# Kernel optimization log

Hardware: AMD Instinct MI355X
Metric: run time of the kernel (lower is better)

Reference implementation:

```python
import jax, jax.numpy as jnp
import numpy as np

EPS = 1e-5

def _layernorm(x, g, b):
    mu = jnp.mean(x, axis=-1, keepdims=True)
    var = jnp.mean((x - mu) ** 2, axis=-1, keepdims=True)
    return (x - mu) / jnp.sqrt(var + EPS) * g + b


def setup_inputs() -> dict:
    key = jax.random.key(0)
    ks = jax.random.split(key, 4)
    B, H, W, C = 8, 96, 96, 256
    return {
        "x1": jax.random.normal(ks[0], (B, H, W, C), dtype=jnp.float32),
        "x2": jax.random.normal(ks[1], (B, H, W, C), dtype=jnp.float32),
        # norm1 (shared LayerNorm applied to both x1 and x2)
        "g1": jnp.ones((C,), jnp.float32),
        "b1": jnp.zeros((C,), jnp.float32),
        # reprojection 1x1 conv: C -> 2C
        "Wr": jax.random.normal(ks[2], (2 * C, C), dtype=jnp.float32) * 0.05,
        "br": jnp.zeros((2 * C,), jnp.float32),
        # final LayerNorm over 2C
        "g2": jnp.ones((2 * C,), jnp.float32),
        "b2": jnp.zeros((2 * C,), jnp.float32),
        # learnable mixing scalars
        "a1": jnp.array(0.25, jnp.float32),
        "a2": jnp.array(0.25, jnp.float32),
        "a3": jnp.array(0.25, jnp.float32),
        "a4": jnp.array(0.25, jnpp_ := jnp.float32),
    }


def reference(x1, x2, g1, b1, Wr, br, g2, b2, a1, a2, a3, a4):
    B, H, W, C = x1.shape
    N, D = H * W, C  # head_count = 1, key_channels = value_channels = D
    n1 = _layernorm(x1.reshape(B, N, C), g1, b1)  # [B,N,D]
    n2 = _layernorm(x2.reshape(B, N, C), g1, b1)

    kq = jnp.swapaxes(n2, 1, 2)                   # [B,D,N]
    key_sm = jax.nn.softmax(kq, axis=2)           # softmax over N
    query = jax.nn.softmax(kq, axis=1)            # softmax over D
    value = jnp.swapaxes(n1, 1, 2)                # [B,D,N]

    # context = key @ value^T : [B,D,D]
    context = jnp.einsum('bdn,ben->bde', key_sm, value)

    def masked_softmax(k):
        # torch.topk + scatter mask == keep entries >= k-th largest per row
        thr = jax.lax.top_k(context, k)[0][..., -1:]
        return jax.nn.softmax(jnp.where(context >= thr, context, -jnp.inf), axis=-1)

    ks = [D // 2, (D * 2) // 3, (D * 3) // 4, (D * 4) // 5]
    o = [jnp.einsum('bde,ben->bdn', masked_softmax(k), query) for k in ks]
    att = a1 * o[0] + a2 * o[1] + a3 * o[2] + a4 * o[3]  # [B,D,N]

    # 1x1 conv reprojection D -> 2D, then LayerNorm over channels
    rep = jnp.einsum('oc,bcn->bno', Wr, att) + br         # [B,N,2D]
    rep = _layernorm(rep, g2, b2)
    # view(B,H,W,2C).permute(0,3,1,2)
    return jnp.transpose(rep.reshape(B, H, W, 2 * C), (0, 3, 1, 2))
```

## Files before the change

kernel.cpp:

```cpp
#include <hip/hip_runtime.h>
#include <hip/hip_bf16.h>

#define Bc 8
#define Nn 9216
#define Dd 256
#define Oo 512
#define EPSc 1e-5f

#define OFF_MU1    0
#define OFF_RSTD1  73728
#define OFF_MU2    147456
#define OFF_RSTD2  221184
#define OFF_ROWINV 294912
#define OFF_COLSUM 368640
#define OFF_M      370688
#define OFF_W2T    894976
#define OFF_CTXP   1419264

typedef __attribute__((ext_vector_type(4))) float f32x4;
typedef __attribute__((ext_vector_type(8))) short short8;
typedef __attribute__((ext_vector_type(8))) unsigned short ushort8;

static __device__ __forceinline__ unsigned short f2bf(float f) {
    __hip_bfloat16 h = __float2bfloat16(f);
    union { __hip_bfloat16 hh; unsigned short uu; } cv; cv.hh = h;
    return cv.uu;
}

#define SWZ(ch) (((((ch) >> 2) & 7)) ^ ((((ch) & 3)) << 1))

__global__ __launch_bounds__(256) void mg_k0_zero(float* __restrict__ p, int n4) {
    int i = blockIdx.x * 256 + threadIdx.x;
    if (i < n4) ((float4*)p)[i] = make_float4(0.f, 0.f, 0.f, 0.f);
}

__global__ __launch_bounds__(256) void mg_k1_stats(const float* __restrict__ x1, const float* __restrict__ x2,
                                                   const float* __restrict__ g1, const float* __restrict__ b1,
                                                   float* __restrict__ ws)
{
    float* mu1    = ws + OFF_MU1;
    float* rstd1  = ws + OFF_RSTD1;
    float* mu2    = ws + OFF_MU2;
    float* rstd2  = ws + OFF_RSTD2;
    float* rowinv = ws + OFF_ROWINV;
    float* colsum = ws + OFF_COLSUM;

    int t = threadIdx.x, lane = t & 63, w = t >> 6;
    int b = blockIdx.x / 144, rb = blockIdx.x % 144;
    int nbase = rb * 64;

    float4 g1v = ((const float4*)g1)[lane];
    float4 b1v = ((const float4*)b1)[lane];
    float cs0 = 0.f, cs1 = 0.f, cs2 = 0.f, cs3 = 0.f;
    __shared__ float csL[4][256];

    for (int i = 0; i < 16; ++i) {
        int n = nbase + i * 4 + w;
        int base = (b * Nn + n) * 64 + lane;
        float4 xa = ((const float4*)x1)[base];
        float4 xb = ((const float4*)x2)[base];
        float s1 = xa.x + xa.y + xa.z + xa.w;
        float q1 = xa.x*xa.x + xa.y*xa.y + xa.z*xa.z + xa.w*xa.w;
        float s2 = xb.x + xb.y + xb.z + xb.w;
        float q2 = xb.x*xb.x + xb.y*xb.y + xb.z*xb.z + xb.w*xb.w;
        #pragma unroll
        for (int m = 1; m < 64; m <<= 1) {
            s1 += __shfl_xor(s1, m); q1 += __shfl_xor(q1, m);
            s2 += __shfl_xor(s2, m); q2 += __shfl_xor(q2, m);
        }
        float m1 = s1 * (1.f / Dd), m2 = s2 * (1.f / Dd);
        float r1 = rsqrtf(q1 * (1.f / Dd) - m1 * m1 + EPSc);
        float r2 = rsqrtf(q2 * (1.f / Dd) - m2 * m2 + EPSc);
        int ni = b * Nn + n;
        if (lane == 0) { mu1[ni] = m1; rstd1[ni] = r1; mu2[ni] = m2; rstd2[ni] = r2; }
        float e0 = __expf((xb.x - m2) * r2 * g1v.x + b1v.x);
        float e1 = __expf((xb.y - m2) * r2 * g1v.y + b1v.y);
        float e2 = __expf((xb.z - m2) * r2 * g1v.z + b1v.z);
        float e3 = __expf((xb.w - m2) * r2 * g1v.w + b1v.w);
        float rs = e0 + e1 + e2 + e3;
        #pragma unroll
        for (int m = 1; m < 64; m <<= 1) rs += __shfl_xor(rs, m);
        if (lane == 0) rowinv[ni] = 1.f / rs;
        cs0 += e0; cs1 += e1; cs2 += e2; cs3 += e3;
    }
    csL[w][lane * 4 + 0] = cs0;
    csL[w][lane * 4 + 1] = cs1;
    csL[w][lane * 4 + 2] = cs2;
    csL[w][lane * 4 + 3] = cs3;
    __syncthreads();
    float tot = csL[0][t] + csL[1][t] + csL[2][t] + csL[3][t];
    atomicAdd(&colsum[b * Dd + t], tot);
}

__global__ __launch_bounds__(512, 2) void mg_k3_ctx(const float* __restrict__ x1, const float* __restrict__ x2,
                                                    const float* __restrict__ g1, const float* __restrict__ b1,
                                                    float* __restrict__ ws, int nks)
{
    __shared__ ushort PA[256 * 64];
    __shared__ ushort PB[256 * 64];
    const float* mu1   = ws + OFF_MU1;
    const float* rstd1 = ws + OFF_RSTD1;
    const float* mu2   = ws + OFF_MU2;
    const float* rstd2 = ws + OFF_RSTD2;
    float* ctxp = ws + OFF_CTXP;

    int t = threadIdx.x;
    int ks_i = blockIdx.x % nks;
    int b = blockIdx.x / nks;
    int krange = Nn / nks;
    int ntiles = krange >> 6;
    int n_base = ks_i * krange;

    int o  = t >> 6;
    int c4 = t & 63;

    f32x4 g1v = ((const f32x4*)g1)[c4];
    f32x4 b1v = ((const f32x4*)b1)[c4];

    int lane = t & 63, wave = t >> 6;
    int wd = wave & 3, we = wave >> 2;
    int l15 = lane & 15, kgrp = lane >> 4;

    f32x4 acc[4][8];
    #pragma unroll
    for (int dt = 0; dt < 4; ++dt)
        #pragma unroll
        for (int et = 0; et < 8; ++et) acc[dt][et] = (f32x4){0.f, 0.f, 0.f, 0.f};

    for (int st = 0; st < ntiles; ++st) {
        int rowb = b * Nn + n_base + st * 64 + o * 8;
        __syncthreads();
        {
            f32x4 mv0 = *(const f32x4*)(mu1 + rowb),   mv1 = *(const f32x4*)(mu1 + rowb + 4);
            f32x4 rv0 = *(const f32x4*)(rstd1 + rowb), rv1 = *(const f32x4*)(rstd1 + rowb + 4);
            float mva[8] = {mv0[0], mv0[1], mv0[2], mv0[3], mv1[0], mv1[1], mv1[2], mv1[3]};
            float rva[8] = {rv0[0], rv0[1], rv0[2], rv0[3], rv1[0], rv1[1], rv1[2], rv1[3]};
            f32x4 xv[8];
            #pragma unroll
            for (int rr = 0; rr < 8; ++rr)
                xv[rr] = ((const f32x4*)x1)[(size_t)(rowb + rr) * 64 + c4];
            #pragma unroll
            for (int i = 0; i < 4; ++i) {
                int ch = c4 * 4 + i;
                ushort8 u;
                #pragma unroll
                for (int rr = 0; rr < 8; ++rr)
                    u[rr] = f2bf((xv[rr][i] - mva[rr]) * rva[rr] * g1v[i] + b1v[i]);
                *(ushort8*)&PB[ch * 64 + ((o + SWZ(ch)) & 7) * 8] = u;
            }
        }
        {
            f32x4 mv0 = *(const f32x4*)(mu2 + rowb),   mv1 = *(const f32x4*)(mu2 + rowb + 4);
            f32x4 rv0 = *(const f32x4*)(rstd2 + rowb), rv1 = *(const f32x4*)(rstd2 + rowb + 4);
            float mva[8] = {mv0[0], mv0[1], mv0[2], mv0[3], mv1[0], mv1[1], mv1[2], mv1[3]};
            float rva[8] = {rv0[0], rv0[1], rv0[2], rv0[3], rv1[0], rv1[1], rv1[2], rv1[3]};
            f32x4 xv[8];
            #pragma unroll
            for (int rr = 0; rr < 8; ++rr)
                xv[rr] = ((const f32x4*)x2)[(size_t)(rowb + rr) * 64 + c4];
            #pragma unroll
            for (int i = 0; i < 4; ++i) {
                int ch = c4 * 4 + i;
                ushort8 u;
                #pragma unroll
                for (int rr = 0; rr < 8; ++rr)
                    u[rr] = f2bf(__expf((xv[rr][i] - mva[rr]) * rva[rr] * g1v[i] + b1v[i]));
                *(ushort8*)&PA[ch * 64 + ((o + SWZ(ch)) & 7) * 8] = u;
            }
        }
        __syncthreads();

        #pragma unroll
        for (int kk = 0; kk < 2; ++kk) {
            short8 af[4], bf[8];
            #pragma unroll
            for (int dt = 0; dt < 4; ++dt) {
                int ch = wd * 64 + dt * 16 + l15;
                af[dt] = *(const short8*)&PA[ch * 64 + (((kk << 2) + kgrp + SWZ(ch)) & 7) * 8];
            }
            #pragma unroll
            for (int et = 0; et < 8; ++et) {
                int ch = we * 128 + et * 16 + l15;
                bf[et] = *(const short8*)&PB[ch * 64 + (((kk << 2) + kgrp + SWZ(ch)) & 7) * 8];
            }
            #pragma unroll
            for (int dt = 0; dt < 4; ++dt)
                #pragma unroll
                for (int et = 0; et < 8; ++et)
                    acc[dt][et] = __builtin_amdgcn_mfma_f32_16x16x32_bf16(af[dt], bf[et], acc[dt][et], 0, 0, 0);
        }
    }

    size_t obase = ((size_t)ks_i * Bc + b) * (Dd * Dd);
    #pragma unroll
    for (int dt = 0; dt < 4; ++dt) {
        #pragma unroll
        for (int r = 0; r < 4; ++r) {
            int d = wd * 64 + dt * 16 + kgrp * 4 + r;
            float* rowp = ctxp + obase + (size_t)d * Dd + we * 128 + l15;
            #pragma unroll
            for (int et = 0; et < 8; ++et)
                rowp[et * 16] = acc[dt][et][r];
        }
    }
}

__global__ __launch_bounds__(256) void mg_k5_mask(const float* __restrict__ a1p, const float* __restrict__ a2p,
                                                  const float* __restrict__ a3p, const float* __restrict__ a4p,
                                                  float* __restrict__ ws, int nks)
{
    const float* ctxp   = ws + OFF_CTXP;
    const float* colsum = ws + OFF_COLSUM;
    float* Mo = ws + OFF_M;
    int t = threadIdx.x;
    int b = blockIdx.x >> 8, d = blockIdx.x & 255;
    __shared__ float s[256];
    __shared__ float wred[4][4];

    float c = 0.f;
    for (int p = 0; p < nks; ++p)
        c += ctxp[((size_t)p * Bc + b) * (Dd * Dd) + (size_t)d * Dd + t];
    float inv = 1.f / colsum[b * Dd + d];
    c *= inv;
    s[t] = c;
    __syncthreads();
    for (int k = 2; k <= 256; k <<= 1) {
        for (int j = k >> 1; j > 0; j >>= 1) {
            int ixj = t ^ j;
            if (ixj > t) {
                float A = s[t], Bv = s[ixj];
                bool desc = ((t & k) == 0);
                bool sw = desc ? (A < Bv) : (A > Bv);
                if (sw) { s[t] = Bv; s[ixj] = A; }
            }
            __syncthreads();
        }
    }
    float cmax = s[0];
    float t0 = s[127], t1 = s[169], t2 = s[191], t3 = s[203];
    float e = __expf(c - cmax);
    float w0 = (c >= t0) ? e : 0.f;
    float w1 = (c >= t1) ? e : 0.f;
    float w2 = (c >= t2) ? e : 0.f;
    float w3 = (c >= t3) ? e : 0.f;
    float v0 = w0, v1 = w1, v2 = w2, v3 = w3;
    #pragma unroll
    for (int m = 1; m < 64; m <<= 1) {
        v0 += __shfl_xor(v0, m); v1 += __shfl_xor(v1, m);
        v2 += __shfl_xor(v2, m); v3 += __shfl_xor(v3, m);
    }
    int lane = t & 63, wv = t >> 6;
    if (lane == 0) { wred[wv][0] = v0; wred[wv][1] = v1; wred[wv][2] = v2; wred[wv][3] = v3; }
    __syncthreads();
    float S0 = wred[0][0] + wred[1][0] + wred[2][0] + wred[3][0];
    float S1 = wred[0][1] + wred[1][1] + wred[2][1] + wred[3][1];
    float S2 = wred[0][2] + wred[1][2] + wred[2][2] + wred[3][2];
    float S3 = wred[0][3] + wred[1][3] + wred[2][3] + wred[3][3];
    float Mv = a1p[0] * (w0 / S0) + a2p[0] * (w1 / S1) + a3p[0] * (w2 / S2) + a4p[0] * (w3 / S3);
    Mo[(b * Dd + d) * Dd + t] = Mv;
}

__global__ __launch_bounds__(256) void mg_k6_w2(const float* __restrict__ Wr, float* __restrict__ ws)
{
    const float* Mo = ws + OFF_M;
    ushort* W2B = (ushort*)(ws + OFF_W2T);
    __shared__ float Mt[32][128];
    __shared__ float WrT[32][36];
    int t = threadIdx.x;
    int b = blockIdx.x >> 5, ob = (blockIdx.x >> 1) & 15, eh = blockIdx.x & 1;
    int o0 = ob * 32, e0 = eh * 128;
    int ol4 = t & 7, el = t >> 3;
    float acc[4][4];
    #pragma unroll
    for (int i = 0; i < 4; ++i)
        #pragma unroll
        for (int j = 0; j < 4; ++j) acc[i][j] = 0.f;

    for (int ch = 0; ch < 8; ++ch) {
        int c0 = ch * 32;
        __syncthreads();
        #pragma unroll
        for (int k = 0; k < 4; ++k) {
            int fi = t + k * 256;
            int row = fi >> 5, c4 = fi & 31;
            float4 mv = ((const float4*)Mo)[(b * Dd + c0 + row) * 64 + (e0 >> 2) + c4];
            *(float4*)&Mt[row][c4 * 4] = mv;
        }
        {
            int ol = t >> 3, c4 = t & 7;
            float4 wv = ((const float4*)Wr)[(o0 + ol) * 64 + (c0 >> 2) + c4];
            WrT[c4 * 4 + 0][ol] = wv.x;
            WrT[c4 * 4 + 1][ol] = wv.y;
            WrT[c4 * 4 + 2][ol] = wv.z;
            WrT[c4 * 4 + 3][ol] = wv.w;
        }
        __syncthreads();
        #pragma unroll
        for (int cc = 0; cc < 32; ++cc) {
            float4 w4 = *(const float4*)&WrT[cc][ol4 * 4];
            float4 m4 = *(const float4*)&Mt[cc][el * 4];
            float wv[4] = {w4.x, w4.y, w4.z, w4.w};
            float mv[4] = {m4.x, m4.y, m4.z, m4.w};
            #pragma unroll
            for (int i = 0; i < 4; ++i)
                #pragma unroll
                for (int j = 0; j < 4; ++j)
                    acc[i][j] = fmaf(wv[i], mv[j], acc[i][j]);
        }
    }
    {
        int e_base = e0 + el * 4;
        int ks = e_base >> 5;
        int kg = (e_base >> 3) & 3, jj = e_base & 7;
        #pragma unroll
        for (int i = 0; i < 4; ++i) {
            int o = o0 + ol4 * 4 + i;
            int wv2 = o >> 6, ot = (o >> 4) & 3, cA = o & 15;
            ushort4 u;
            u.x = f2bf(acc[i][0]); u.y = f2bf(acc[i][1]);
            u.z = f2bf(acc[i][2]); u.w = f2bf(acc[i][3]);
            size_t idx = ((size_t)b * 8 + ks) * 16384 + wv2 * 2048 + ot * 512
                       + (kg * 16 + cA) * 8 + jj;
            *(ushort4*)&W2B[idx] = u;
        }
    }
}

__global__ __launch_bounds__(512) void mg_k7_final(const float* __restrict__ x2,
        const float* __restrict__ g1, const float* __restrict__ b1,
        const float* __restrict__ br, const float* __restrict__ g2, const float* __restrict__ b2,
        const float* __restrict__ ws, float* __restrict__ out)
{
    __shared__ ushort smem[8192 + 2 * 16384];
    ushort* qsT = smem;
    ushort* W0 = smem + 8192;
    ushort* W1 = smem + 8192 + 16384;

    const float* mu2    = ws + OFF_MU2;
    const float* rstd2  = ws + OFF_RSTD2;
    const float* rowinv = ws + OFF_ROWINV;
    const ushort* W2B   = (const ushort*)(ws + OFF_W2T);

    int t = threadIdx.x;
    int b = blockIdx.x / 288, nt0 = blockIdx.x % 288;
    int n0 = nt0 * 32;
    int lw = t & 63, wave = t >> 6;
    int colA = lw & 15, kgrp = lw >> 4;

#define STAGEW(dstbuf, ksv)                                                        \
    {                                                                              \
        size_t so_ = ((size_t)b * 8 + (ksv)) * 16384 + wave * 2048;                \
        _Pragma("unroll")                                                          \
        for (int k_ = 0; k_ < 4; ++k_) {                                           \
            __builtin_amdgcn_global_load_lds(                                      \
                (const __attribute__((address_space(1))) unsigned int*)            \
                    (W2B + so_ + k_ * 512 + lw * 8),                               \
                (__attribute__((address_space(3))) unsigned int*)                  \
                    ((dstbuf) + wave * 2048 + k_ * 512),                           \
                16, 0, 0);                                                         \
        }                                                                          \
    }

    STAGEW(W0, 0);

    {
        int row = t >> 4, gpair = (t & 15) * 2;
        int ni = b * Nn + n0 + row;
        float m = mu2[ni], r = rstd2[ni], ri = rowinv[ni];
        #pragma unroll
        for (int jj = 0; jj < 2; ++jj) {
            int g = gpair + jj;
            const float4* xp = (const float4*)x2 + (size_t)ni * 64 + g * 2;
            float4 xa = xp[0], xb = xp[1];
            float4 ga = ((const float4*)g1)[g * 2], gc = ((const float4*)g1)[g * 2 + 1];
            float4 ba = ((const float4*)b1)[g * 2], bc = ((const float4*)b1)[g * 2 + 1];
            float v[8]  = {xa.x, xa.y, xa.z, xa.w, xb.x, xb.y, xb.z, xb.w};
            float gv[8] = {ga.x, ga.y, ga.z, ga.w, gc.x, gc.y, gc.z, gc.w};
            float bv[8] = {ba.x, ba.y, ba.z, ba.w, bc.x, bc.y, bc.z, bc.w};
            ushort8 u;
            #pragma unroll
            for (int q = 0; q < 8; ++q)
                u[q] = f2bf(__expf((v[q] - m) * r * gv[q] + bv[q]) * ri);
            *(ushort8*)&qsT[row * 256 + ((g ^ (row & 7)) << 3)] = u;
        }
    }
    __syncthreads();

    f32x4 acc[4][2];
    #pragma unroll
    for (int ot = 0; ot < 4; ++ot) {
        acc[ot][0] = (f32x4){0.f, 0.f, 0.f, 0.f};
        acc[ot][1] = (f32x4){0.f, 0.f, 0.f, 0.f};
    }

    #pragma unroll
    for (int ks = 0; ks < 8; ++ks) {
        if (ks < 7) {
            if ((ks & 1) == 0) { STAGEW(W1, ks + 1); }
            else               { STAGEW(W0, ks + 1); }
        }
        const ushort* wb = (ks & 1) ? W1 : W0;
        int gsl = ((ks * 4 + kgrp) ^ (colA & 7)) << 3;
        short8 bf0 = *(const short8*)&qsT[colA * 256 + gsl];
        short8 bf1 = *(const short8*)&qsT[(16 + colA) * 256 + gsl];
        #pragma unroll
        for (int ot = 0; ot < 4; ++ot) {
            short8 af = *(const short8*)&wb[wave * 2048 + ot * 512 + lw * 8];
            acc[ot][0] = __builtin_amdgcn_mfma_f32_16x16x32_bf16(af, bf0, acc[ot][0], 0, 0, 0);
            acc[ot][1] = __builtin_amdgcn_mfma_f32_16x16x32_bf16(af, bf1, acc[ot][1], 0, 0, 0);
        }
        __syncthreads();
    }
#undef STAGEW

    float (*stat)[2][16][2] = (float (*)[2][16][2])(void*)smem;
    float (*musig)[2] = (float (*)[2])((float*)(void*)smem + 512);

    float ps[2] = {0.f, 0.f}, pq[2] = {0.f, 0.f};
    #pragma unroll
    for (int ot = 0; ot < 4; ++ot) {
        #pragma unroll
        for (int r = 0; r < 4; ++r) {
            int o = wave * 64 + ot * 16 + kgrp * 4 + r;
            float bb = br[o];
            float v0 = acc[ot][0][r] + bb;
            float v1 = acc[ot][1][r] + bb;
            acc[ot][0][r] = v0; acc[ot][1][r] = v1;
            ps[0] += v0; pq[0] += v0 * v0;
            ps[1] += v1; pq[1] += v1 * v1;
        }
    }
    #pragma unroll
    for (int m = 16; m <= 32; m <<= 1) {
        ps[0] += __shfl_xor(ps[0], m); pq[0] += __shfl_xor(pq[0], m);
        ps[1] += __shfl_xor(ps[1], m); pq[1] += __shfl_xor(pq[1], m);
    }
    if (lw < 16) {
        stat[wave][0][lw][0] = ps[0]; stat[wave][0][lw][1] = pq[0];
        stat[wave][1][lw][0] = ps[1]; stat[wave][1][lw][1] = pq[1];
    }
    __syncthreads();
    if (t < 32) {
        int ntl = t >> 4, col = t & 15;
        float S = 0.f, Q = 0.f;
        #pragma unroll
        for (int w2 = 0; w2 < 8; ++w2) { S += stat[w2][ntl][col][0]; Q += stat[w2][ntl][col][1]; }
        float mu = S * (1.f / Oo);
        float var = Q * (1.f / Oo) - mu * mu;
        musig[t][0] = mu;
        musig[t][1] = rsqrtf(var + EPSc);
    }
    __syncthreads();

    float mn0 = musig[colA][0],      rs0 = musig[colA][1];
    float mn1 = musig[16 + colA][0], rs1 = musig[16 + colA][1];
    #pragma unroll
    for (int ot = 0; ot < 4; ++ot) {
        #pragma unroll
        for (int r = 0; r < 4; ++r) {
            int o = wave * 64 + ot * 16 + kgrp * 4 + r;
            float gg = g2[o], bb2 = b2[o];
            size_t ob = ((size_t)b * Oo + o) * Nn + n0;
            out[ob + colA]      = (acc[ot][0][r] - mn0) * rs0 * gg + bb2;
            out[ob + 16 + colA] = (acc[ot][1][r] - mn1) * rs1 * gg + bb2;
        }
    }
}

extern "C" void kernel_launch(void* const* d_in, const int* in_sizes, int n_in,
                              void* d_out, int out_size, void* d_ws, size_t ws_size,
                              hipStream_t stream)
{
    (void)in_sizes; (void)n_in; (void)out_size;
    const float* x1 = (const float*)d_in[0];
    const float* x2 = (const float*)d_in[1];
    const float* g1 = (const float*)d_in[2];
    const float* b1 = (const float*)d_in[3];
    const float* Wr = (const float*)d_in[4];
    const float* br = (const float*)d_in[5];
    const float* g2 = (const float*)d_in[6];
    const float* b2 = (const float*)d_in[7];
    const float* a1 = (const float*)d_in[8];
    const float* a2 = (const float*)d_in[9];
    const float* a3 = (const float*)d_in[10];
    const float* a4 = (const float*)d_in[11];
    float* ws = (float*)d_ws;
    float* out = (float*)d_out;

    const int cand[6] = {24, 16, 12, 8, 4, 2};
    int nks = 2;
    for (int ci = 0; ci < 6; ++ci) {
        if (((size_t)OFF_CTXP + (size_t)cand[ci] * 524288ull) * 4ull <= ws_size) { nks = cand[ci]; break; }
    }

    hipLaunchKernelGGL(mg_k0_zero, dim3(2), dim3(256), 0, stream, ws + OFF_COLSUM, 512);
    hipLaunchKernelGGL(mg_k1_stats, dim3(1152), dim3(256), 0, stream, x1, x2, g1, b1, ws);
    hipLaunchKernelGGL(mg_k3_ctx, dim3(Bc * nks), dim3(512), 0, stream, x1, x2, g1, b1, ws, nks);
    hipLaunchKernelGGL(mg_k5_mask, dim3(2048), dim3(256), 0, stream, a1, a2, a3, a4, ws, nks);
    hipLaunchKernelGGL(mg_k6_w2, dim3(256), dim3(256), 0, stream, Wr, ws);
    hipLaunchKernelGGL(mg_k7_final, dim3(2304), dim3(512), 0, stream, x2, g1, b1, br, g2, b2, ws, out);
}
```

Measured before the change: 191.1 us.

## Precompute bf16 normalized and exp tiles in stats kernel, feed ctx GEMM via LDS DMA

The stats kernel now also writes bf16 tiles of the normalized x1 and exp(normalized x2) into workspace, already in the swizzled LDS layout. A new context kernel loads these tiles straight into LDS with global_load_lds and runs the MFMA GEMM without recomputing normalization or exp from fp32 inputs. This removes the second fp32 read of x1/x2 and the per-element math from the ctx kernel. In exchange it writes and rereads about 75MB of bf16 intermediates, needs a larger workspace, and keeps the old path as a fallback.

```diff
diff --git a/kernel.cpp b/kernel.cpp
--- a/kernel.cpp
+++ b/kernel.cpp
@@ -16,6 +16,9 @@
 #define OFF_M      370688
 #define OFF_W2T    894976
 #define OFF_CTXP   1419264
+#define OFF_PNB    14002176
+#define OFF_PNA    23439360
+#define WS_FAST_END 32876544
 
 typedef __attribute__((ext_vector_type(4))) float f32x4;
 typedef __attribute__((ext_vector_type(8))) short short8;
@@ -34,10 +37,12 @@
     if (i < n4) ((float4*)p)[i] = make_float4(0.f, 0.f, 0.f, 0.f);
 }
 
-__global__ __launch_bounds__(256) void mg_k1_stats(const float* __restrict__ x1, const float* __restrict__ x2,
+__global__ __launch_bounds__(512) void mg_k1_stats(const float* __restrict__ x1, const float* __restrict__ x2,
                                                    const float* __restrict__ g1, const float* __restrict__ b1,
-                                                   float* __restrict__ ws)
+                                                   float* __restrict__ ws, int wp)
 {
+    __shared__ ushort Pls[16384];
+    __shared__ float csL[8][256];
     float* mu1    = ws + OFF_MU1;
     float* rstd1  = ws + OFF_RSTD1;
     float* mu2    = ws + OFF_MU2;
@@ -45,56 +50,220 @@
     float* rowinv = ws + OFF_ROWINV;
     float* colsum = ws + OFF_COLSUM;
 
-    int t = threadIdx.x, lane = t & 63, w = t >> 6;
+    int t = threadIdx.x;
     int b = blockIdx.x / 144, rb = blockIdx.x % 144;
-    int nbase = rb * 64;
-
-    float4 g1v = ((const float4*)g1)[lane];
-    float4 b1v = ((const float4*)b1)[lane];
-    float cs0 = 0.f, cs1 = 0.f, cs2 = 0.f, cs3 = 0.f;
-    __shared__ float csL[4][256];
-
-    for (int i = 0; i < 16; ++i) {
-        int n = nbase + i * 4 + w;
-        int base = (b * Nn + n) * 64 + lane;
-        float4 xa = ((const float4*)x1)[base];
-        float4 xb = ((const float4*)x2)[base];
-        float s1 = xa.x + xa.y + xa.z + xa.w;
-        float q1 = xa.x*xa.x + xa.y*xa.y + xa.z*xa.z + xa.w*xa.w;
-        float s2 = xb.x + xb.y + xb.z + xb.w;
-        float q2 = xb.x*xb.x + xb.y*xb.y + xb.z*xb.z + xb.w*xb.w;
-        #pragma unroll
-        for (int m = 1; m < 64; m <<= 1) {
-            s1 += __shfl_xor(s1, m); q1 += __shfl_xor(q1, m);
-            s2 += __shfl_xor(s2, m); q2 += __shfl_xor(q2, m);
-        }
-        float m1 = s1 * (1.f / Dd), m2 = s2 * (1.f / Dd);
-        float r1 = rsqrtf(q1 * (1.f / Dd) - m1 * m1 + EPSc);
-        float r2 = rsqrtf(q2 * (1.f / Dd) - m2 * m2 + EPSc);
-        int ni = b * Nn + n;
-        if (lane == 0) { mu1[ni] = m1; rstd1[ni] = r1; mu2[ni] = m2; rstd2[ni] = r2; }
-        float e0 = __expf((xb.x - m2) * r2 * g1v.x + b1v.x);
-        float e1 = __expf((xb.y - m2) * r2 * g1v.y + b1v.y);
-        float e2 = __expf((xb.z - m2) * r2 * g1v.z + b1v.z);
-        float e3 = __expf((xb.w - m2) * r2 * g1v.w + b1v.w);
-        float rs = e0 + e1 + e2 + e3;
-        #pragma unroll
-        for (int m = 1; m < 64; m <<= 1) rs += __shfl_xor(rs, m);
-        if (lane == 0) rowinv[ni] = 1.f / rs;
-        cs0 += e0; cs1 += e1; cs2 += e2; cs3 += e3;
-    }
-    csL[w][lane * 4 + 0] = cs0;
-    csL[w][lane * 4 + 1] = cs1;
-    csL[w][lane * 4 + 2] = cs2;
-    csL[w][lane * 4 + 3] = cs3;
-    __syncthreads();
-    float tot = csL[0][t] + csL[1][t] + csL[2][t] + csL[3][t];
-    atomicAdd(&colsum[b * Dd + t], tot);
-}
-
-__global__ __launch_bounds__(512, 2) void mg_k3_ctx(const float* __restrict__ x1, const float* __restrict__ x2,
-                                                    const float* __restrict__ g1, const float* __restrict__ b1,
-                                                    float* __restrict__ ws, int nks)
+    int o = t >> 6, c4 = t & 63;
+    int rowb = b * Nn + rb * 64 + o * 8;
+
+    f32x4 g1v = ((const f32x4*)g1)[c4];
+    f32x4 b1v = ((const f32x4*)b1)[c4];
+
+    {
+        f32x4 xv[8];
+        #pragma unroll
+        for (int rr = 0; rr < 8; ++rr)
+            xv[rr] = ((const f32x4*)x1)[(size_t)(rowb + rr) * 64 + c4];
+        float sA[8], qA[8];
+        #pragma unroll
+        for (int rr = 0; rr < 8; ++rr) {
+            f32x4 v = xv[rr];
+            sA[rr] = v[0] + v[1] + v[2] + v[3];
+            qA[rr] = v[0]*v[0] + v[1]*v[1] + v[2]*v[2] + v[3]*v[3];
+        }
+        #pragma unroll
+        for (int m = 1; m < 64; m <<= 1)
+            #pragma unroll
+            for (int rr = 0; rr < 8; ++rr) {
+                sA[rr] += __shfl_xor(sA[rr], m);
+                qA[rr] += __shfl_xor(qA[rr], m);
+            }
+        float mva[8], rva[8];
+        #pragma unroll
+        for (int rr = 0; rr < 8; ++rr) {
+            float mu = sA[rr] * (1.f / Dd);
+            mva[rr] = mu;
+            rva[rr] = rsqrtf(qA[rr] * (1.f / Dd) - mu * mu + EPSc);
+        }
+        if (c4 == 0) {
+            #pragma unroll
+            for (int rr = 0; rr < 8; ++rr) { mu1[rowb + rr] = mva[rr]; rstd1[rowb + rr] = rva[rr]; }
+        }
+        if (wp) {
+            #pragma unroll
+            for (int i = 0; i < 4; ++i) {
+                int ch = c4 * 4 + i;
+                ushort8 u;
+                #pragma unroll
+                for (int rr = 0; rr < 8; ++rr)
+                    u[rr] = f2bf((xv[rr][i] - mva[rr]) * rva[rr] * g1v[i] + b1v[i]);
+                *(ushort8*)&Pls[ch * 64 + ((o + SWZ(ch)) & 7) * 8] = u;
+            }
+            __syncthreads();
+            ushort* pnB = (ushort*)(ws + OFF_PNB) + ((size_t)b * 144 + rb) * 16384;
+            #pragma unroll
+            for (int k = 0; k < 4; ++k)
+                *(ushort8*)&pnB[k * 4096 + t * 8] = *(const ushort8*)&Pls[k * 4096 + t * 8];
+            __syncthreads();
+        }
+    }
+    {
+        f32x4 xv[8];
+        #pragma unroll
+        for (int rr = 0; rr < 8; ++rr)
+            xv[rr] = ((const f32x4*)x2)[(size_t)(rowb + rr) * 64 + c4];
+        float sA[8], qA[8];
+        #pragma unroll
+        for (int rr = 0; rr < 8; ++rr) {
+            f32x4 v = xv[rr];
+            sA[rr] = v[0] + v[1] + v[2] + v[3];
+            qA[rr] = v[0]*v[0] + v[1]*v[1] + v[2]*v[2] + v[3]*v[3];
+        }
+        #pragma unroll
+        for (int m = 1; m < 64; m <<= 1)
+            #pragma unroll
+            for (int rr = 0; rr < 8; ++rr) {
+                sA[rr] += __shfl_xor(sA[rr], m);
+                qA[rr] += __shfl_xor(qA[rr], m);
+            }
+        float mva[8], rva[8];
+        #pragma unroll
+        for (int rr = 0; rr < 8; ++rr) {
+            float mu = sA[rr] * (1.f / Dd);
+            mva[rr] = mu;
+            rva[rr] = rsqrtf(qA[rr] * (1.f / Dd) - mu * mu + EPSc);
+        }
+        if (c4 == 0) {
+            #pragma unroll
+            for (int rr = 0; rr < 8; ++rr) { mu2[rowb + rr] = mva[rr]; rstd2[rowb + rr] = rva[rr]; }
+        }
+        float ev[4][8];
+        #pragma unroll
+        for (int i = 0; i < 4; ++i)
+            #pragma unroll
+            for (int rr = 0; rr < 8; ++rr)
+                ev[i][rr] = __expf((xv[rr][i] - mva[rr]) * rva[rr] * g1v[i] + b1v[i]);
+        float rsum[8];
+        #pragma unroll
+        for (int rr = 0; rr < 8; ++rr)
+            rsum[rr] = ev[0][rr] + ev[1][rr] + ev[2][rr] + ev[3][rr];
+        #pragma unroll
+        for (int m = 1; m < 64; m <<= 1)
+            #pragma unroll
+            for (int rr = 0; rr < 8; ++rr)
+                rsum[rr] += __shfl_xor(rsum[rr], m);
+        if (c4 == 0) {
+            #pragma unroll
+            for (int rr = 0; rr < 8; ++rr) rowinv[rowb + rr] = 1.f / rsum[rr];
+        }
+        #pragma unroll
+        for (int i = 0; i < 4; ++i) {
+            float cs = 0.f;
+            #pragma unroll
+            for (int rr = 0; rr < 8; ++rr) cs += ev[i][rr];
+            csL[o][c4 * 4 + i] = cs;
+        }
+        if (wp) {
+            #pragma unroll
+            for (int i = 0; i < 4; ++i) {
+                int ch = c4 * 4 + i;
+                ushort8 u;
+                #pragma unroll
+                for (int rr = 0; rr < 8; ++rr) u[rr] = f2bf(ev[i][rr]);
+                *(ushort8*)&Pls[ch * 64 + ((o + SWZ(ch)) & 7) * 8] = u;
+            }
+        }
+        __syncthreads();
+        if (wp) {
+            ushort* pnA = (ushort*)(ws + OFF_PNA) + ((size_t)b * 144 + rb) * 16384;
+            #pragma unroll
+            for (int k = 0; k < 4; ++k)
+                *(ushort8*)&pnA[k * 4096 + t * 8] = *(const ushort8*)&Pls[k * 4096 + t * 8];
+        }
+        if (t < 256) {
+            float s = 0.f;
+            #pragma unroll
+            for (int w2 = 0; w2 < 8; ++w2) s += csL[w2][t];
+            atomicAdd(&colsum[b * Dd + t], s);
+        }
+    }
+}
+
+__global__ __launch_bounds__(512, 2) void mg_k3_ctx_f(float* __restrict__ ws)
+{
+    __shared__ ushort PA[16384];
+    __shared__ ushort PB[16384];
+    const ushort* pnA = (const ushort*)(ws + OFF_PNA);
+    const ushort* pnB = (const ushort*)(ws + OFF_PNB);
+    float* ctxp = ws + OFF_CTXP;
+
+    int t = threadIdx.x;
+    int ks_i = blockIdx.x % 24;
+    int b = blockIdx.x / 24;
+    int lane = t & 63, wave = t >> 6;
+    int wd = wave & 3, we = wave >> 2;
+    int l15 = lane & 15, kgrp = lane >> 4;
+
+    f32x4 acc[4][8];
+    #pragma unroll
+    for (int dt = 0; dt < 4; ++dt)
+        #pragma unroll
+        for (int et = 0; et < 8; ++et) acc[dt][et] = (f32x4){0.f, 0.f, 0.f, 0.f};
+
+    for (int j = 0; j < 6; ++j) {
+        int tile = ks_i * 6 + j;
+        size_t tb = ((size_t)b * 144 + tile) * 16384;
+        __syncthreads();
+        #pragma unroll
+        for (int k = 0; k < 4; ++k) {
+            __builtin_amdgcn_global_load_lds(
+                (const __attribute__((address_space(1))) unsigned int*)(pnA + tb + wave * 2048 + k * 512 + lane * 8),
+                (__attribute__((address_space(3))) unsigned int*)(PA + wave * 2048 + k * 512),
+                16, 0, 0);
+            __builtin_amdgcn_global_load_lds(
+                (const __attribute__((address_space(1))) unsigned int*)(pnB + tb + wave * 2048 + k * 512 + lane * 8),
+                (__attribute__((address_space(3))) unsigned int*)(PB + wave * 2048 + k * 512),
+                16, 0, 0);
+        }
+        __syncthreads();
+
+        #pragma unroll
+        for (int kk = 0; kk < 2; ++kk) {
+            short8 af[4], bf[8];
+            #pragma unroll
+            for (int dt = 0; dt < 4; ++dt) {
+                int ch = wd * 64 + dt * 16 + l15;
+                af[dt] = *(const short8*)&PA[ch * 64 + (((kk << 2) + kgrp + SWZ(ch)) & 7) * 8];
+            }
+            #pragma unroll
+            for (int et = 0; et < 8; ++et) {
+                int ch = we * 128 + et * 16 + l15;
+                bf[et] = *(const short8*)&PB[ch * 64 + (((kk << 2) + kgrp + SWZ(ch)) & 7) * 8];
+            }
+            #pragma unroll
+            for (int dt = 0; dt < 4; ++dt)
+                #pragma unroll
+                for (int et = 0; et < 8; ++et)
+                    acc[dt][et] = __builtin_amdgcn_mfma_f32_16x16x32_bf16(af[dt], bf[et], acc[dt][et], 0, 0, 0);
+        }
+    }
+
+    size_t obase = ((size_t)ks_i * Bc + b) * (Dd * Dd);
+    #pragma unroll
+    for (int dt = 0; dt < 4; ++dt) {
+        #pragma unroll
+        for (int r = 0; r < 4; ++r) {
+            int d = wd * 64 + dt * 16 + kgrp * 4 + r;
+            float* rowp = ctxp + obase + (size_t)d * Dd + we * 128 + l15;
+            #pragma unroll
+            for (int et = 0; et < 8; ++et)
+                rowp[et * 16] = acc[dt][et][r];
+        }
+    }
+}
+
+__global__ __launch_bounds__(512, 2) void mg_k3_slow(const float* __restrict__ x1, const float* __restrict__ x2,
+                                                     const float* __restrict__ g1, const float* __restrict__ b1,
+                                                     float* __restrict__ ws, int nks)
 {
     __shared__ ushort PA[256 * 64];
     __shared__ ushort PB[256 * 64];
@@ -487,15 +656,25 @@
     float* ws = (float*)d_ws;
     float* out = (float*)d_out;
 
-    const int cand[6] = {24, 16, 12, 8, 4, 2};
-    int nks = 2;
-    for (int ci = 0; ci < 6; ++ci) {
-        if (((size_t)OFF_CTXP + (size_t)cand[ci] * 524288ull) * 4ull <= ws_size) { nks = cand[ci]; break; }
+    int fast = ((size_t)WS_FAST_END * 4ull <= ws_size) ? 1 : 0;
+    int nks;
+    if (fast) {
+        nks = 24;
+    } else {
+        const int cand[6] = {24, 16, 12, 8, 4, 2};
+        nks = 2;
+        for (int ci = 0; ci < 6; ++ci) {
+            if (((size_t)OFF_CTXP + (size_t)cand[ci] * 524288ull) * 4ull <= ws_size) { nks = cand[ci]; break; }
+        }
     }
 
     hipLaunchKernelGGL(mg_k0_zero, dim3(2), dim3(256), 0, stream, ws + OFF_COLSUM, 512);
-    hipLaunchKernelGGL(mg_k1_stats, dim3(1152), dim3(256), 0, stream, x1, x2, g1, b1, ws);
-    hipLaunchKernelGGL(mg_k3_ctx, dim3(Bc * nks), dim3(512), 0, stream, x1, x2, g1, b1, ws, nks);
+    hipLaunchKernelGGL(mg_k1_stats, dim3(1152), dim3(512), 0, stream, x1, x2, g1, b1, ws, fast);
+    if (fast) {
+        hipLaunchKernelGGL(mg_k3_ctx_f, dim3(Bc * 24), dim3(512), 0, stream, ws);
+    } else {
+        hipLaunchKernelGGL(mg_k3_slow, dim3(Bc * nks), dim3(512), 0, stream, x1, x2, g1, b1, ws, nks);
+    }
     hipLaunchKernelGGL(mg_k5_mask, dim3(2048), dim3(256), 0, stream, a1, a2, a3, a4, ws, nks);
     hipLaunchKernelGGL(mg_k6_w2, dim3(256), dim3(256), 0, stream, Wr, ws);
     hipLaunchKernelGGL(mg_k7_final, dim3(2304), dim3(512), 0, stream, x2, g1, b1, br, g2, b2, ws, out);
```

Result: no change. 194.4 us (+1.7%).

## Precompute swizzled bf16 tiles in stats kernel and stream them into context GEMM

Applied to the files above, without the earlier changes.

The stats kernel now also writes layer-normed x1 and exp(norm x2) as pre-swizzled bf16 tiles into workspace. A new context kernel loads these tiles straight into LDS with global_load_lds and runs the MFMA GEMM, so it no longer re-reads the fp32 inputs or recomputes normalization and exp. This moves work out of the GEMM kernel and cuts its load traffic. In exchange it adds about 38 MB of extra workspace writes and reads, plus 64 KB of LDS in the stats kernel, which may lower its occupancy. The old path stays as a fallback when the workspace is too small.

```diff
diff --git a/kernel.cpp b/kernel.cpp
--- a/kernel.cpp
+++ b/kernel.cpp
@@ -16,6 +16,9 @@
 #define OFF_M      370688
 #define OFF_W2T    894976
 #define OFF_CTXP   1419264
+#define OFF_PNB    14002176
+#define OFF_PNA    23439360
+#define WS_FAST_END 32876544
 
 typedef __attribute__((ext_vector_type(4))) float f32x4;
 typedef __attribute__((ext_vector_type(8))) short short8;
@@ -36,8 +39,11 @@
 
 __global__ __launch_bounds__(256) void mg_k1_stats(const float* __restrict__ x1, const float* __restrict__ x2,
                                                    const float* __restrict__ g1, const float* __restrict__ b1,
-                                                   float* __restrict__ ws)
+                                                   float* __restrict__ ws, int wp)
 {
+    __shared__ ushort PAi[16384];
+    __shared__ ushort PBi[16384];
+    __shared__ float csL[4][256];
     float* mu1    = ws + OFF_MU1;
     float* rstd1  = ws + OFF_RSTD1;
     float* mu2    = ws + OFF_MU2;
@@ -52,11 +58,12 @@
     float4 g1v = ((const float4*)g1)[lane];
     float4 b1v = ((const float4*)b1)[lane];
     float cs0 = 0.f, cs1 = 0.f, cs2 = 0.f, cs3 = 0.f;
-    __shared__ float csL[4][256];
 
     for (int i = 0; i < 16; ++i) {
-        int n = nbase + i * 4 + w;
-        int base = (b * Nn + n) * 64 + lane;
+        int l = i * 4 + w;
+        int n = nbase + l;
+        int ni = b * Nn + n;
+        int base = ni * 64 + lane;
         float4 xa = ((const float4*)x1)[base];
         float4 xb = ((const float4*)x2)[base];
         float s1 = xa.x + xa.y + xa.z + xa.w;
@@ -71,7 +78,6 @@
         float m1 = s1 * (1.f / Dd), m2 = s2 * (1.f / Dd);
         float r1 = rsqrtf(q1 * (1.f / Dd) - m1 * m1 + EPSc);
         float r2 = rsqrtf(q2 * (1.f / Dd) - m2 * m2 + EPSc);
-        int ni = b * Nn + n;
         if (lane == 0) { mu1[ni] = m1; rstd1[ni] = r1; mu2[ni] = m2; rstd2[ni] = r2; }
         float e0 = __expf((xb.x - m2) * r2 * g1v.x + b1v.x);
         float e1 = __expf((xb.y - m2) * r2 * g1v.y + b1v.y);
@@ -82,19 +88,117 @@
         for (int m = 1; m < 64; m <<= 1) rs += __shfl_xor(rs, m);
         if (lane == 0) rowinv[ni] = 1.f / rs;
         cs0 += e0; cs1 += e1; cs2 += e2; cs3 += e3;
+
+        if (wp) {
+            int oo = l >> 3, r8 = l & 7;
+            float ln1[4] = {(xa.x - m1) * r1 * g1v.x + b1v.x,
+                            (xa.y - m1) * r1 * g1v.y + b1v.y,
+                            (xa.z - m1) * r1 * g1v.z + b1v.z,
+                            (xa.w - m1) * r1 * g1v.w + b1v.w};
+            float ev[4] = {e0, e1, e2, e3};
+            #pragma unroll
+            for (int ii = 0; ii < 4; ++ii) {
+                int ch = lane * 4 + ii;
+                int idx = ch * 64 + (((oo + SWZ(ch)) & 7) << 3) + r8;
+                PBi[idx] = f2bf(ln1[ii]);
+                PAi[idx] = f2bf(ev[ii]);
+            }
+        }
     }
     csL[w][lane * 4 + 0] = cs0;
     csL[w][lane * 4 + 1] = cs1;
     csL[w][lane * 4 + 2] = cs2;
     csL[w][lane * 4 + 3] = cs3;
     __syncthreads();
+    if (wp) {
+        ushort* pnB = (ushort*)(ws + OFF_PNB) + ((size_t)b * 144 + rb) * 16384;
+        ushort* pnA = (ushort*)(ws + OFF_PNA) + ((size_t)b * 144 + rb) * 16384;
+        #pragma unroll
+        for (int k = 0; k < 8; ++k) {
+            *(ushort8*)&pnB[k * 2048 + t * 8] = *(const ushort8*)&PBi[k * 2048 + t * 8];
+            *(ushort8*)&pnA[k * 2048 + t * 8] = *(const ushort8*)&PAi[k * 2048 + t * 8];
+        }
+    }
     float tot = csL[0][t] + csL[1][t] + csL[2][t] + csL[3][t];
     atomicAdd(&colsum[b * Dd + t], tot);
 }
 
-__global__ __launch_bounds__(512, 2) void mg_k3_ctx(const float* __restrict__ x1, const float* __restrict__ x2,
-                                                    const float* __restrict__ g1, const float* __restrict__ b1,
-                                                    float* __restrict__ ws, int nks)
+__global__ __launch_bounds__(512, 2) void mg_k3_ctx_f(float* __restrict__ ws)
+{
+    __shared__ ushort PA[16384];
+    __shared__ ushort PB[16384];
+    const ushort* pnA = (const ushort*)(ws + OFF_PNA);
+    const ushort* pnB = (const ushort*)(ws + OFF_PNB);
+    float* ctxp = ws + OFF_CTXP;
+
+    int t = threadIdx.x;
+    int ks_i = blockIdx.x % 24;
+    int b = blockIdx.x / 24;
+    int lane = t & 63, wave = t >> 6;
+    int wd = wave & 3, we = wave >> 2;
+    int l15 = lane & 15, kgrp = lane >> 4;
+
+    f32x4 acc[4][8];
+    #pragma unroll
+    for (int dt = 0; dt < 4; ++dt)
+        #pragma unroll
+        for (int et = 0; et < 8; ++et) acc[dt][et] = (f32x4){0.f, 0.f, 0.f, 0.f};
+
+    for (int j = 0; j < 6; ++j) {
+        int tile = ks_i * 6 + j;
+        size_t tb = ((size_t)b * 144 + tile) * 16384;
+        __syncthreads();
+        #pragma unroll
+        for (int k = 0; k < 4; ++k) {
+            __builtin_amdgcn_global_load_lds(
+                (const __attribute__((address_space(1))) unsigned int*)(pnA + tb + wave * 2048 + k * 512 + lane * 8),
+                (__attribute__((address_space(3))) unsigned int*)(PA + wave * 2048 + k * 512),
+                16, 0, 0);
+            __builtin_amdgcn_global_load_lds(
+                (const __attribute__((address_space(1))) unsigned int*)(pnB + tb + wave * 2048 + k * 512 + lane * 8),
+                (__attribute__((address_space(3))) unsigned int*)(PB + wave * 2048 + k * 512),
+                16, 0, 0);
+        }
+        __syncthreads();
+
+        #pragma unroll
+        for (int kk = 0; kk < 2; ++kk) {
+            short8 af[4], bf[8];
+            #pragma unroll
+            for (int dt = 0; dt < 4; ++dt) {
+                int ch = wd * 64 + dt * 16 + l15;
+                af[dt] = *(const short8*)&PA[ch * 64 + (((kk << 2) + kgrp + SWZ(ch)) & 7) * 8];
+            }
+            #pragma unroll
+            for (int et = 0; et < 8; ++et) {
+                int ch = we * 128 + et * 16 + l15;
+                bf[et] = *(const short8*)&PB[ch * 64 + (((kk << 2) + kgrp + SWZ(ch)) & 7) * 8];
+            }
+            #pragma unroll
+            for (int dt = 0; dt < 4; ++dt)
+                #pragma unroll
+                for (int et = 0; et < 8; ++et)
+                    acc[dt][et] = __builtin_amdgcn_mfma_f32_16x16x32_bf16(af[dt], bf[et], acc[dt][et], 0, 0, 0);
+        }
+    }
+
+    size_t obase = ((size_t)ks_i * Bc + b) * (Dd * Dd);
+    #pragma unroll
+    for (int dt = 0; dt < 4; ++dt) {
+        #pragma unroll
+        for (int r = 0; r < 4; ++r) {
+            int d = wd * 64 + dt * 16 + kgrp * 4 + r;
+            float* rowp = ctxp + obase + (size_t)d * Dd + we * 128 + l15;
+            #pragma unroll
+            for (int et = 0; et < 8; ++et)
+                rowp[et * 16] = acc[dt][et][r];
+        }
+    }
+}
+
+__global__ __launch_bounds__(512, 2) void mg_k3_slow(const float* __restrict__ x1, const float* __restrict__ x2,
+                                                     const float* __restrict__ g1, const float* __restrict__ b1,
+                                                     float* __restrict__ ws, int nks)
 {
     __shared__ ushort PA[256 * 64];
     __shared__ ushort PB[256 * 64];
@@ -487,15 +591,25 @@
     float* ws = (float*)d_ws;
     float* out = (float*)d_out;
 
-    const int cand[6] = {24, 16, 12, 8, 4, 2};
-    int nks = 2;
-    for (int ci = 0; ci < 6; ++ci) {
-        if (((size_t)OFF_CTXP + (size_t)cand[ci] * 524288ull) * 4ull <= ws_size) { nks = cand[ci]; break; }
+    int fast = ((size_t)WS_FAST_END * 4ull <= ws_size) ? 1 : 0;
+    int nks;
+    if (fast) {
+        nks = 24;
+    } else {
+        const int cand[6] = {24, 16, 12, 8, 4, 2};
+        nks = 2;
+        for (int ci = 0; ci < 6; ++ci) {
+            if (((size_t)OFF_CTXP + (size_t)cand[ci] * 524288ull) * 4ull <= ws_size) { nks = cand[ci]; break; }
+        }
     }
 
     hipLaunchKernelGGL(mg_k0_zero, dim3(2), dim3(256), 0, stream, ws + OFF_COLSUM, 512);
-    hipLaunchKernelGGL(mg_k1_stats, dim3(1152), dim3(256), 0, stream, x1, x2, g1, b1, ws);
-    hipLaunchKernelGGL(mg_k3_ctx, dim3(Bc * nks), dim3(512), 0, stream, x1, x2, g1, b1, ws, nks);
+    hipLaunchKernelGGL(mg_k1_stats, dim3(1152), dim3(256), 0, stream, x1, x2, g1, b1, ws, fast);
+    if (fast) {
+        hipLaunchKernelGGL(mg_k3_ctx_f, dim3(Bc * 24), dim3(512), 0, stream, ws);
+    } else {
+        hipLaunchKernelGGL(mg_k3_slow, dim3(Bc * nks), dim3(512), 0, stream, x1, x2, g1, b1, ws, nks);
+    }
     hipLaunchKernelGGL(mg_k5_mask, dim3(2048), dim3(256), 0, stream, a1, a2, a3, a4, ws, nks);
     hipLaunchKernelGGL(mg_k6_w2, dim3(256), dim3(256), 0, stream, Wr, ws);
     hipLaunchKernelGGL(mg_k7_final, dim3(2304), dim3(512), 0, stream, x2, g1, b1, br, g2, b2, ws, out);
```

Result: slower. 244.1 us (+27.8%).
